# Kernel tuning notes

Measured on AMD Instinct MI355X. Metric: run time of the kernel, lower is better.

## Reference

```python
import jax, jax.numpy as jnp
import numpy as np
from jax import lax

SHIFT_SIZE = 5
PAD = SHIFT_SIZE // 2


def _shift(xn, axis):
    """xn: (B, C, Hp, Wp, Dp) zero-padded volume. Split channels into
    SHIFT_SIZE chunks and roll each chunk by shift in [-PAD, PAD] along `axis`."""
    chunks = jnp.split(xn, SHIFT_SIZE, axis=1)
    shifted = [jnp.roll(c, s, axis=axis) for c, s in zip(chunks, range(-PAD, PAD + 1))]
    return jnp.concatenate(shifted, axis=1)


def _shift_tokens(x, H, W, D, axis):
    """x: (B, N, C) tokens -> shifted tokens (B, N, C). axis=2 shifts H, axis=3 shifts W."""
    B, N, C = x.shape
    xn = x.transpose(0, 2, 1).reshape(B, C, H, W, D)
    xn = jnp.pad(xn, ((0, 0), (0, 0), (PAD, PAD), (PAD, PAD), (PAD, PAD)))
    xs = _shift(xn, axis)
    xs = xs[:, :, PAD:PAD + H, PAD:PAD + W, PAD:PAD + D]
    return xs.reshape(B, C, N).transpose(0, 2, 1)


def setup_inputs() -> dict:
    key = jax.random.key(0)
    ks = jax.random.split(key, 4)
    B, H, W, D = 2, 32, 32, 32
    N = H * W * D
    Cin, Ch = 160, 640
    return {
        "x": jax.random.normal(ks[0], (B, N, Cin), jnp.float32),
        "fc1_w": jax.random.normal(ks[1], (Ch, Cin), jnp.float32) * 0.02,
        "fc1_b": jnp.zeros((Ch,), jnp.float32),
        "dw_w": jax.random.normal(ks[2], (Ch, 1, 3, 3, 3), jnp.float32) * (2.0 / 27.0) ** 0.5,
        "dw_b": jnp.zeros((Ch,), jnp.float32),
        "fc2_w": jax.random.normal(ks[3], (Cin, Ch), jnp.float32) * 0.02,
        "fc2_b": jnp.zeros((Cin,), jnp.float32),
        "H": H, "W": W, "D": D,
    }


def reference(x, fc1_w, fc1_b, dw_w, dw_b, fc2_w, fc2_b, H, W, D):
    B, N, Cin = x.shape
    Ch = fc1_w.shape[0]
    # shift block 1: roll along H (axis 2)
    xs = _shift_tokens(x, H, W, D, axis=2)
    # fc1
    h = jnp.einsum('bnc,hc->bnh', xs, fc1_w) + fc1_b  # (B, N, Ch)
    # depthwise 3x3x3 conv
    hv = h.transpose(0, 2, 1).reshape(B, Ch, H, W, D)
    hv = lax.conv_general_dilated(
        hv, dw_w, window_strides=(1, 1, 1), padding='SAME',
        feature_group_count=Ch,
        dimension_numbers=('NCDHW', 'OIDHW', 'NCDHW'))
    hv = hv + dw_b[None, :, None, None, None]
    hv = jax.nn.gelu(hv, approximate=False)
    h = hv.reshape(B, Ch, N).transpose(0, 2, 1)
    # shift block 2: roll along W (axis 3)
    hs = _shift_tokens(h, H, W, D, axis=3)
    # fc2
    out = jnp.einsum('bnh,oh->bno', hs, fc2_w) + fc2_b  # (B, N, Cin)
    return out
```

## Files before the change

kernel.cpp:

```cpp
#include <hip/hip_runtime.h>
#include <hip/hip_bf16.h>
#include <hip/hip_fp16.h>
#include <math.h>

#define DEVI __device__ __forceinline__

typedef _Float16 f16;
typedef f16 f16x2 __attribute__((ext_vector_type(2)));
typedef f16 f16x4 __attribute__((ext_vector_type(4)));
typedef f16 f16x8 __attribute__((ext_vector_type(8)));
typedef float f32x4 __attribute__((ext_vector_type(4)));

constexpr int Bb = 2, Hh = 32, Ww = 32, Dd = 32;
constexpr int Nn = Hh * Ww * Dd;
constexpr int BN = Bb * Nn;
constexpr int CIN = 160, CHH = 640;
constexpr int PD = 34;
constexpr int PT = PD * PD * PD;

constexpr size_t W1_OFF  = 0;
constexpr size_t W2_OFF  = W1_OFF + (size_t)CHH * CIN * 2;
constexpr size_t WTH_OFF = W2_OFF + (size_t)CIN * CHH * 2;
constexpr size_t ZP_OFF  = WTH_OFF + 34816;
constexpr size_t U_OFF   = 458752;
constexpr size_t H1P_OFF = U_OFF + (size_t)BN * CHH * 2;

DEVI void async16(const void* g, void* l) {
  __builtin_amdgcn_global_load_lds(
      (const __attribute__((address_space(1))) void*)g,
      (__attribute__((address_space(3))) void*)l, 16, 0, 0);
}

DEVI f16x8 gelu8(f16x8 xa) {
  const __half2 C1 = __float2half2_rn(2.3022078f);
  const __half2 C2 = __float2half2_rn(0.102943324f);
  const __half2 ONE = __float2half2_rn(1.0f);
  f16x8 out;
#pragma unroll
  for (int j = 0; j < 8; j += 2) {
    __half2 xv = __builtin_bit_cast(__half2, f16x2{xa[j], xa[j + 1]});
    __half2 x2 = __hmul2(xv, xv);
    __half2 t  = __hfma2(x2, C2, C1);
    __half2 u  = __hmul2(xv, t);
    __half2 e  = h2exp2(u);
    __half2 r  = h2rcp(__hadd2(e, ONE));
    __half2 g  = __hsub2(xv, __hmul2(xv, r));
    f16x2 gg = __builtin_bit_cast(f16x2, g);
    out[j] = gg[0]; out[j + 1] = gg[1];
  }
  return out;
}

constexpr int PREPW_BLOCKS = 876;
constexpr int NSHELL = 13072;
constexpr int SHELL_BLOCKS = (NSHELL * 80 + 255) / 256;

__global__ __launch_bounds__(256) void k_prep(const float* __restrict__ fc1w,
                                              const float* __restrict__ fc2w,
                                              const float* __restrict__ dww,
                                              f16* __restrict__ w1h,
                                              f16* __restrict__ w2h,
                                              f16* __restrict__ wTh,
                                              unsigned* __restrict__ zp,
                                              f16* __restrict__ h1p) {
  const int bid = blockIdx.x;
  const int tid = threadIdx.x;
  if (bid < PREPW_BLOCKS) {
    int i = bid * 256 + tid;
    const int NW = CHH * CIN;
    if (i < NW) {
      w1h[i] = (f16)fc1w[i];
    } else if (i < 2 * NW) {
      w2h[i - NW] = (f16)fc2w[i - NW];
    } else if (i < 2 * NW + 27 * CHH) {
      int j = i - 2 * NW;
      int ch = j / 27, tap = j % 27;
      wTh[tap * CHH + ch] = (f16)dww[j];
    } else if (i < 2 * NW + 27 * CHH + 2048) {
      zp[i - (2 * NW + 27 * CHH)] = 0u;
    }
    return;
  }
  int g = (bid - PREPW_BLOCKS) * 256 + tid;
  int t = g / 80;
  int c = g - t * 80;
  if (t >= NSHELL) return;
  int b, hp, wp, dp;
  if (t < 4624) {
    int i = t;
    b = i / 2312; i -= b * 2312;
    int f = i / 1156; i -= f * 1156;
    hp = f ? PD - 1 : 0;
    wp = i / 34; dp = i - (i / 34) * 34;
  } else if (t < 8976) {
    int i = t - 4624;
    b = i / 2176; i -= b * 2176;
    int f = i / 1088; i -= f * 1088;
    wp = f ? PD - 1 : 0;
    hp = 1 + i / 34; dp = i - (i / 34) * 34;
  } else {
    int i = t - 8976;
    b = i / 2048; i -= b * 2048;
    int f = i / 1024; i -= f * 1024;
    dp = f ? PD - 1 : 0;
    hp = 1 + i / 32; wp = 1 + (i & 31);
  }
  size_t p = ((size_t)(b * PD + hp) * PD + wp) * PD + dp;
  f16x8 z = {};
  *(f16x8*)&h1p[p * CHH + c * 8] = z;
}

__global__ __launch_bounds__(256) void k_gemm1(const float* __restrict__ x,
                                               const f16* __restrict__ w1h,
                                               const float* __restrict__ fc1b,
                                               f16* __restrict__ h1p) {
  constexpr int LDA = 168;
  __shared__ f16 lsA[128 * LDA];
  __shared__ f16 lsB[128 * 32];
  const int tid = threadIdx.x;
  const int lane = tid & 63, wave = tid >> 6;
  const int row0 = blockIdx.x * 128;
  const int wr = wave >> 1, wc = wave & 1;
  const int rl = lane & 15, kb = (lane >> 4) * 8;

#pragma unroll
  for (int i = 0; i < 20; ++i) {
    int c = i * 256 + tid;
    int row = c / 40;
    int q = c - row * 40;
    int ch0 = q * 4;
    int ks = ch0 >> 5;
    int s = ks - 2;
    int t = row0 + row;
    int h = (t >> 10) & 31;
    int hs = h - s;
    float4 v = {0.f, 0.f, 0.f, 0.f};
    if (hs >= 0 && hs < 32)
      v = *(const float4*)&x[(long)(t - s * 1024) * CIN + ch0];
    f16x4 o4;
    o4[0] = (f16)v.x; o4[1] = (f16)v.y; o4[2] = (f16)v.z; o4[3] = (f16)v.w;
    *(f16x4*)&lsA[row * LDA + ch0] = o4;
  }
  __syncthreads();

  for (int nt = 0; nt < 5; ++nt) {
    const int col0 = nt * 128;
    f32x4 acc[4][4] = {};
    for (int ks = 0; ks < 5; ++ks) {
#pragma unroll
      for (int issue = 0; issue < 2; ++issue) {
        int c = issue * 256 + tid;
        int br = c >> 2;
        int ju = (c & 3) ^ (br & 3);
        const f16* src = w1h + (size_t)(col0 + br) * CIN + ks * 32 + ju * 8;
        async16(src, (char*)lsB + issue * 4096 + wave * 1024);
      }
      __syncthreads();
      f16x8 af[4], bfr[4];
#pragma unroll
      for (int mi = 0; mi < 4; ++mi)
        af[mi] = *(const f16x8*)&lsA[(wr * 64 + mi * 16 + rl) * LDA + ks * 32 + kb];
#pragma unroll
      for (int ni = 0; ni < 4; ++ni) {
        int row = wc * 64 + ni * 16 + rl;
        int u = (lane >> 4) ^ (rl & 3);
        bfr[ni] = *(const f16x8*)&lsB[row * 32 + u * 8];
      }
#pragma unroll
      for (int mi = 0; mi < 4; ++mi)
#pragma unroll
        for (int ni = 0; ni < 4; ++ni)
          acc[mi][ni] = __builtin_amdgcn_mfma_f32_16x16x32_f16(af[mi], bfr[ni], acc[mi][ni], 0, 0, 0);
      __syncthreads();
    }
    const int rq = lane >> 4;
#pragma unroll
    for (int mi = 0; mi < 4; ++mi) {
      int rowq = row0 + wr * 64 + mi * 16 + rq * 4;
      int bq = rowq >> 15;
      int nq = rowq & 32767;
      int hq = nq >> 10, wq = (nq >> 5) & 31, dq = nq & 31;
      size_t pos = (size_t)((bq * PD + hq + 1) * PD + (wq + 1)) * PD + (dq + 1);
      f16* dst0 = h1p + pos * CHH;
#pragma unroll
      for (int ni = 0; ni < 4; ++ni) {
        int col = col0 + wc * 64 + ni * 16 + rl;
        float bias = fc1b[col];
#pragma unroll
        for (int r = 0; r < 4; ++r)
          dst0[(size_t)r * CHH + col] = (f16)(acc[mi][ni][r] + bias);
      }
    }
  }
}

__global__ __launch_bounds__(256) void k_conv(const f16* __restrict__ h1p,
                                              const f16* __restrict__ wTh,
                                              const float* __restrict__ dwb,
                                              f16* __restrict__ h2h) {
  __shared__ f16 lw[27 * 64];
  __shared__ f16 lb[64];
  const int tid = threadIdx.x;
  const int bid = blockIdx.x;
  const int wg = (bid & 7) * 320 + (bid >> 3);
  const int cg = wg % 10;
  const int oct = wg / 10;
#pragma unroll
  for (int i = 0; i < 7; ++i) {
    int idx = i * 256 + tid;
    if (idx < 27 * 64) lw[idx] = wTh[(idx >> 6) * CHH + cg * 64 + (idx & 63)];
  }
  if (tid < 64) lb[tid] = (f16)dwb[cg * 64 + tid];
  __syncthreads();

  const int lane = tid & 63, wave = tid >> 6;
  const int L0 = oct * 8 + wave * 2;
  const int c8 = lane & 7, dq = lane >> 3;
  const int d0 = dq * 4;
  const int ch0 = cg * 64 + c8 * 8;
  const int w0 = L0 & 31, h = (L0 >> 5) & 31, b = L0 >> 10;

  const size_t cidx = (size_t)((b * PD + h) * PD + w0) * PD + d0;
  const f16* base = h1p + cidx * CHH + ch0;

  f16x8 acc0[4], acc1[4];
  {
    f16x8 binit = *(const f16x8*)&lb[c8 * 8];
#pragma unroll
    for (int o = 0; o < 4; ++o) { acc0[o] = binit; acc1[o] = binit; }
  }

#pragma unroll
  for (int kz = 0; kz < 3; ++kz) {
    f16x8 wt[3][3];
#pragma unroll
    for (int ky = 0; ky < 3; ++ky)
#pragma unroll
      for (int kx = 0; kx < 3; ++kx)
        wt[ky][kx] = *(const f16x8*)&lw[((kz * 9 + ky * 3 + kx) << 6) + c8 * 8];
#pragma unroll
    for (int py = 0; py < 4; ++py) {
      const f16* pb = base + (size_t)(kz * PD + py) * PD * CHH;
      f16x8 v[6];
#pragma unroll
      for (int j = 0; j < 6; ++j)
        v[j] = *(const f16x8*)(pb + (size_t)j * CHH);
      if (py < 3) {
#pragma unroll
        for (int o = 0; o < 4; ++o)
#pragma unroll
          for (int kx = 0; kx < 3; ++kx)
            acc0[o] = v[o + kx] * wt[py][kx] + acc0[o];
      }
      if (py >= 1) {
#pragma unroll
        for (int o = 0; o < 4; ++o)
#pragma unroll
          for (int kx = 0; kx < 3; ++kx)
            acc1[o] = v[o + kx] * wt[py - 1][kx] + acc1[o];
      }
    }
  }

  const ptrdiff_t ob0 = (ptrdiff_t)(L0 * 32 + d0) * CHH + ch0;
  const ptrdiff_t ob1 = ob0 + (ptrdiff_t)32 * CHH;
#pragma unroll
  for (int o = 0; o < 4; ++o) {
    *(f16x8*)&h2h[ob0 + (ptrdiff_t)o * CHH] = gelu8(acc0[o]);
    *(f16x8*)&h2h[ob1 + (ptrdiff_t)o * CHH] = gelu8(acc1[o]);
  }
}

__global__ __launch_bounds__(256) void k_gemm2(const f16* __restrict__ h2h,
                                               const f16* __restrict__ w2h,
                                               const float* __restrict__ fc2b,
                                               const f16* __restrict__ zp,
                                               float* __restrict__ out) {
  __shared__ f16 lsA[128 * 64];
  __shared__ f16 lsB[160 * 64];
  const int tid = threadIdx.x, lane = tid & 63, wave = tid >> 6;
  const int row0 = blockIdx.x * 128;
  const int rl = lane & 15;

  f32x4 acc[2][10] = {};

  for (int kt = 0; kt < 10; ++kt) {
    __syncthreads();
    const int k0 = kt * 64;
    const int s = (kt >> 1) - 2;
#pragma unroll
    for (int issue = 0; issue < 4; ++issue) {
      int c = issue * 256 + tid;
      int ar = c >> 3;
      int ju = (c & 7) ^ (ar & 7);
      int kc = ju * 8;
      int t = row0 + ar;
      int w = (t >> 5) & 31;
      int wsv = w - s;
      const f16* src;
      if (wsv >= 0 && wsv < 32)
        src = h2h + (size_t)(t - s * 32) * CHH + k0 + kc;
      else
        src = zp + (size_t)(c & 63) * 8;
      async16(src, (char*)lsA + issue * 4096 + wave * 1024);
    }
#pragma unroll
    for (int issue = 0; issue < 5; ++issue) {
      int c = issue * 256 + tid;
      int br = c >> 3;
      int ju = (c & 7) ^ (br & 7);
      const f16* src = w2h + (size_t)br * CHH + k0 + ju * 8;
      async16(src, (char*)lsB + issue * 4096 + wave * 1024);
    }
    __syncthreads();
#pragma unroll
    for (int kk = 0; kk < 2; ++kk) {
      f16x8 af[2], bfr[10];
#pragma unroll
      for (int mi = 0; mi < 2; ++mi) {
        int row = wave * 32 + mi * 16 + rl;
        int u = (kk * 4 + (lane >> 4)) ^ (rl & 7);
        af[mi] = *(const f16x8*)&lsA[row * 64 + u * 8];
      }
#pragma unroll
      for (int ni = 0; ni < 10; ++ni) {
        int row = ni * 16 + rl;
        int u = (kk * 4 + (lane >> 4)) ^ (rl & 7);
        bfr[ni] = *(const f16x8*)&lsB[row * 64 + u * 8];
      }
#pragma unroll
      for (int mi = 0; mi < 2; ++mi)
#pragma unroll
        for (int ni = 0; ni < 10; ++ni)
          acc[mi][ni] = __builtin_amdgcn_mfma_f32_16x16x32_f16(af[mi], bfr[ni], acc[mi][ni], 0, 0, 0);
    }
  }
  const int rq = lane >> 4;
#pragma unroll
  for (int mi = 0; mi < 2; ++mi) {
#pragma unroll
    for (int ni = 0; ni < 10; ++ni) {
      int col = ni * 16 + rl;
      float bias = fc2b[col];
#pragma unroll
      for (int r = 0; r < 4; ++r) {
        int row = row0 + wave * 32 + mi * 16 + rq * 4 + r;
        out[(size_t)row * CIN + col] = acc[mi][ni][r] + bias;
      }
    }
  }
}

extern "C" void kernel_launch(void* const* d_in, const int* in_sizes, int n_in,
                              void* d_out, int out_size, void* d_ws, size_t ws_size,
                              hipStream_t stream) {
  const float* x    = (const float*)d_in[0];
  const float* fc1w = (const float*)d_in[1];
  const float* fc1b = (const float*)d_in[2];
  const float* dww  = (const float*)d_in[3];
  const float* dwb  = (const float*)d_in[4];
  const float* fc2w = (const float*)d_in[5];
  const float* fc2b = (const float*)d_in[6];

  char* ws = (char*)d_ws;
  f16* w1h  = (f16*)(ws + W1_OFF);
  f16* w2h  = (f16*)(ws + W2_OFF);
  f16* wTh  = (f16*)(ws + WTH_OFF);
  f16* zp   = (f16*)(ws + ZP_OFF);
  f16* h2h  = (f16*)(ws + U_OFF);
  f16* h1p  = (f16*)(ws + H1P_OFF);
  float* out = (float*)d_out;

  k_prep<<<PREPW_BLOCKS + SHELL_BLOCKS, 256, 0, stream>>>(
      fc1w, fc2w, dww, w1h, w2h, wTh, (unsigned*)zp, h1p);
  k_gemm1<<<512, 256, 0, stream>>>(x, w1h, fc1b, h1p);
  k_conv<<<2560, 256, 0, stream>>>(h1p, wTh, dwb, h2h);
  k_gemm2<<<512, 256, 0, stream>>>(h2h, w2h, fc2b, zp, out);
}
```

Before: 120.7 us.

## Fuse depthwise conv and GELU into fc2 GEMM A-tile production

Drops the separate depthwise-conv kernel and its intermediate h2h buffer. The fc2 GEMM now computes the shifted conv+GELU activations directly into its LDS A tile, reading from the padded h1p tensor, with shifted-out rows zero-filled. This removes a full write and read of the BN x 640 fp16 intermediate and one launch. In exchange, the conv arithmetic now sits inside the GEMM loop, weights are read from global memory rather than LDS, and the A-tile loads are no longer asynchronous.

```diff
diff --git a/kernel.cpp b/kernel.cpp
--- a/kernel.cpp
+++ b/kernel.cpp
@@ -22,8 +22,7 @@
 constexpr size_t W2_OFF  = W1_OFF + (size_t)CHH * CIN * 2;
 constexpr size_t WTH_OFF = W2_OFF + (size_t)CIN * CHH * 2;
 constexpr size_t ZP_OFF  = WTH_OFF + 34816;
-constexpr size_t U_OFF   = 458752;
-constexpr size_t H1P_OFF = U_OFF + (size_t)BN * CHH * 2;
+constexpr size_t H1P_OFF = 458752;
 
 DEVI void async16(const void* g, void* l) {
   __builtin_amdgcn_global_load_lds(
@@ -194,93 +193,20 @@
   }
 }
 
-__global__ __launch_bounds__(256) void k_conv(const f16* __restrict__ h1p,
-                                              const f16* __restrict__ wTh,
-                                              const float* __restrict__ dwb,
-                                              f16* __restrict__ h2h) {
-  __shared__ f16 lw[27 * 64];
-  __shared__ f16 lb[64];
-  const int tid = threadIdx.x;
-  const int bid = blockIdx.x;
-  const int wg = (bid & 7) * 320 + (bid >> 3);
-  const int cg = wg % 10;
-  const int oct = wg / 10;
-#pragma unroll
-  for (int i = 0; i < 7; ++i) {
-    int idx = i * 256 + tid;
-    if (idx < 27 * 64) lw[idx] = wTh[(idx >> 6) * CHH + cg * 64 + (idx & 63)];
-  }
-  if (tid < 64) lb[tid] = (f16)dwb[cg * 64 + tid];
-  __syncthreads();
-
-  const int lane = tid & 63, wave = tid >> 6;
-  const int L0 = oct * 8 + wave * 2;
-  const int c8 = lane & 7, dq = lane >> 3;
-  const int d0 = dq * 4;
-  const int ch0 = cg * 64 + c8 * 8;
-  const int w0 = L0 & 31, h = (L0 >> 5) & 31, b = L0 >> 10;
-
-  const size_t cidx = (size_t)((b * PD + h) * PD + w0) * PD + d0;
-  const f16* base = h1p + cidx * CHH + ch0;
-
-  f16x8 acc0[4], acc1[4];
-  {
-    f16x8 binit = *(const f16x8*)&lb[c8 * 8];
-#pragma unroll
-    for (int o = 0; o < 4; ++o) { acc0[o] = binit; acc1[o] = binit; }
-  }
-
-#pragma unroll
-  for (int kz = 0; kz < 3; ++kz) {
-    f16x8 wt[3][3];
-#pragma unroll
-    for (int ky = 0; ky < 3; ++ky)
-#pragma unroll
-      for (int kx = 0; kx < 3; ++kx)
-        wt[ky][kx] = *(const f16x8*)&lw[((kz * 9 + ky * 3 + kx) << 6) + c8 * 8];
-#pragma unroll
-    for (int py = 0; py < 4; ++py) {
-      const f16* pb = base + (size_t)(kz * PD + py) * PD * CHH;
-      f16x8 v[6];
-#pragma unroll
-      for (int j = 0; j < 6; ++j)
-        v[j] = *(const f16x8*)(pb + (size_t)j * CHH);
-      if (py < 3) {
-#pragma unroll
-        for (int o = 0; o < 4; ++o)
-#pragma unroll
-          for (int kx = 0; kx < 3; ++kx)
-            acc0[o] = v[o + kx] * wt[py][kx] + acc0[o];
-      }
-      if (py >= 1) {
-#pragma unroll
-        for (int o = 0; o < 4; ++o)
-#pragma unroll
-          for (int kx = 0; kx < 3; ++kx)
-            acc1[o] = v[o + kx] * wt[py - 1][kx] + acc1[o];
-      }
-    }
-  }
-
-  const ptrdiff_t ob0 = (ptrdiff_t)(L0 * 32 + d0) * CHH + ch0;
-  const ptrdiff_t ob1 = ob0 + (ptrdiff_t)32 * CHH;
-#pragma unroll
-  for (int o = 0; o < 4; ++o) {
-    *(f16x8*)&h2h[ob0 + (ptrdiff_t)o * CHH] = gelu8(acc0[o]);
-    *(f16x8*)&h2h[ob1 + (ptrdiff_t)o * CHH] = gelu8(acc1[o]);
-  }
-}
-
-__global__ __launch_bounds__(256) void k_gemm2(const f16* __restrict__ h2h,
-                                               const f16* __restrict__ w2h,
-                                               const float* __restrict__ fc2b,
-                                               const f16* __restrict__ zp,
-                                               float* __restrict__ out) {
+__global__ __launch_bounds__(256) void k_gemm2f(const f16* __restrict__ h1p,
+                                                const f16* __restrict__ wTh,
+                                                const float* __restrict__ dwb,
+                                                const f16* __restrict__ w2h,
+                                                const float* __restrict__ fc2b,
+                                                float* __restrict__ out) {
   __shared__ f16 lsA[128 * 64];
   __shared__ f16 lsB[160 * 64];
   const int tid = threadIdx.x, lane = tid & 63, wave = tid >> 6;
   const int row0 = blockIdx.x * 128;
   const int rl = lane & 15;
+  const int w0 = (row0 >> 5) & 31, h = (row0 >> 10) & 31, b = row0 >> 15;
+  const int c8 = lane & 7, dq = lane >> 3;
+  const int d0 = dq * 4;
 
   f32x4 acc[2][10] = {};
 
@@ -288,22 +214,7 @@
     __syncthreads();
     const int k0 = kt * 64;
     const int s = (kt >> 1) - 2;
-#pragma unroll
-    for (int issue = 0; issue < 4; ++issue) {
-      int c = issue * 256 + tid;
-      int ar = c >> 3;
-      int ju = (c & 7) ^ (ar & 7);
-      int kc = ju * 8;
-      int t = row0 + ar;
-      int w = (t >> 5) & 31;
-      int wsv = w - s;
-      const f16* src;
-      if (wsv >= 0 && wsv < 32)
-        src = h2h + (size_t)(t - s * 32) * CHH + k0 + kc;
-      else
-        src = zp + (size_t)(c & 63) * 8;
-      async16(src, (char*)lsA + issue * 4096 + wave * 1024);
-    }
+
 #pragma unroll
     for (int issue = 0; issue < 5; ++issue) {
       int c = issue * 256 + tid;
@@ -312,7 +223,56 @@
       const f16* src = w2h + (size_t)br * CHH + k0 + ju * 8;
       async16(src, (char*)lsB + issue * 4096 + wave * 1024);
     }
+
+    const int wsrc = w0 + wave - s;
+    const int rbase = wave * 32 + d0;
+    if ((unsigned)wsrc < 32u) {
+      const f16* tb = h1p + ((size_t)((b * PD + h) * PD + wsrc) * PD + d0) * CHH + k0 + c8 * 8;
+      f16x8 cacc[4];
+      {
+        float4 ba = *(const float4*)&dwb[k0 + c8 * 8];
+        float4 bb = *(const float4*)&dwb[k0 + c8 * 8 + 4];
+        f16x8 bi;
+        bi[0] = (f16)ba.x; bi[1] = (f16)ba.y; bi[2] = (f16)ba.z; bi[3] = (f16)ba.w;
+        bi[4] = (f16)bb.x; bi[5] = (f16)bb.y; bi[6] = (f16)bb.z; bi[7] = (f16)bb.w;
+#pragma unroll
+        for (int o = 0; o < 4; ++o) cacc[o] = bi;
+      }
+#pragma unroll
+      for (int kz = 0; kz < 3; ++kz) {
+#pragma unroll
+        for (int ky = 0; ky < 3; ++ky) {
+          const f16* pb = tb + (size_t)(kz * PD + ky) * PD * CHH;
+          f16x8 wt[3];
+#pragma unroll
+          for (int kx = 0; kx < 3; ++kx)
+            wt[kx] = *(const f16x8*)&wTh[(kz * 9 + ky * 3 + kx) * CHH + k0 + c8 * 8];
+          f16x8 v[6];
+#pragma unroll
+          for (int j = 0; j < 6; ++j)
+            v[j] = *(const f16x8*)(pb + (size_t)j * CHH);
+#pragma unroll
+          for (int o = 0; o < 4; ++o)
+#pragma unroll
+            for (int kx = 0; kx < 3; ++kx)
+              cacc[o] = v[o + kx] * wt[kx] + cacc[o];
+        }
+      }
+#pragma unroll
+      for (int o = 0; o < 4; ++o) {
+        int r = rbase + o;
+        *(f16x8*)&lsA[r * 64 + (c8 ^ (r & 7)) * 8] = gelu8(cacc[o]);
+      }
+    } else {
+      f16x8 z = {};
+#pragma unroll
+      for (int o = 0; o < 4; ++o) {
+        int r = rbase + o;
+        *(f16x8*)&lsA[r * 64 + (c8 ^ (r & 7)) * 8] = z;
+      }
+    }
     __syncthreads();
+
 #pragma unroll
     for (int kk = 0; kk < 2; ++kk) {
       f16x8 af[2], bfr[10];
@@ -335,6 +295,7 @@
           acc[mi][ni] = __builtin_amdgcn_mfma_f32_16x16x32_f16(af[mi], bfr[ni], acc[mi][ni], 0, 0, 0);
     }
   }
+
   const int rq = lane >> 4;
 #pragma unroll
   for (int mi = 0; mi < 2; ++mi) {
@@ -367,13 +328,11 @@
   f16* w2h  = (f16*)(ws + W2_OFF);
   f16* wTh  = (f16*)(ws + WTH_OFF);
   f16* zp   = (f16*)(ws + ZP_OFF);
-  f16* h2h  = (f16*)(ws + U_OFF);
   f16* h1p  = (f16*)(ws + H1P_OFF);
   float* out = (float*)d_out;
 
   k_prep<<<PREPW_BLOCKS + SHELL_BLOCKS, 256, 0, stream>>>(
       fc1w, fc2w, dww, w1h, w2h, wTh, (unsigned*)zp, h1p);
   k_gemm1<<<512, 256, 0, stream>>>(x, w1h, fc1b, h1p);
-  k_conv<<<2560, 256, 0, stream>>>(h1p, wTh, dwb, h2h);
-  k_gemm2<<<512, 256, 0, stream>>>(h2h, w2h, fc2b, zp, out);
-}
+  k_gemm2f<<<512, 256, 0, stream>>>(h1p, wTh, dwb, w2h, fc2b, out);
+}
```

After: 196.9 us. 1.63x slower.
